# Kernel tuning notes

Measured on AMD Instinct MI355X. Metric: run time of the kernel, lower is better.

Reference implementation:

```python
import jax, jax.numpy as jnp
import numpy as np

R, C = 30, 56
N = R * C  # 1680
K = 0.005
PRCN = 15
ALPHA = 1.0
BETA = 1.0


def setup_inputs() -> dict:
    key = jax.random.key(0)
    k1, k2 = jax.random.split(key)
    net_in = jax.random.normal(k1, (2 * N,), dtype=jnp.float32)
    # Recurrent connectivity matrix (learned weight in the original, loaded from .mat)
    J = jax.random.normal(k2, (N, N), dtype=jnp.float32) / np.float32(np.sqrt(N))
    return {"net_in": net_in, "J": J}


def reference(net_in, J):
    Iext = net_in[:N].reshape(R, C)
    r0 = net_in[N:2 * N].reshape(R, C)

    def step(r, _):
        # 4-way chunked mm + cat in the original == single matvec J @ r_flat
        temp = (J @ r.reshape(N)).reshape(R, C)
        U = ALPHA * (BETA * temp) + ALPHA * Iext
        sq = jnp.square(0.2 * U)
        recSum = jnp.sum(K * sq)
        # (0.2*U)^2 * (0.04 / recSum) / 0.04  ==  sq / recSum, kept explicit for fidelity
        r_new = sq * (0.04 / recSum) / 0.04
        return r_new, (U, recSum)

    r_last, (Us, sums) = jax.lax.scan(step, r0, None, length=PRCN - 1)
    return Us[-1], sums[-1], r_last
```

## Files before the change

### kernel.cpp

```cpp
#include <hip/hip_runtime.h>


typedef float f32x4 __attribute__((ext_vector_type(4)));

#define N      1680
#define NV4    420
#define NSTEP  14
#define GBLK   105
#define RPB    16
#define RPW    4

__device__ __forceinline__ f32x4 llc_load4(const f32x4* p) {
    f32x4 v;
    asm volatile("global_load_dwordx4 %0, %1, off sc0 sc1\n\t"
                 "s_waitcnt vmcnt(0)"
                 : "=v"(v) : "v"(p) : "memory");
    return v;
}
__device__ __forceinline__ void llc_store4(f32x4* p, f32x4 v) {
    asm volatile("global_store_dwordx4 %0, %1, off sc0 sc1"
                 :: "v"(p), "v"(v) : "memory");
}

__global__ __launch_bounds__(256, 1) void fused_recur(
    const float* __restrict__ J,
    const float* __restrict__ net_in,
    float* __restrict__ out,
    float* __restrict__ ws)
{
    __shared__ f32x4 r_lds[NV4];
    __shared__ float sred[4];

    f32x4* bufs = (f32x4*)ws;

    const int tid  = threadIdx.x;
    const int lane = tid & 63;
    const int wave = tid >> 6;
    const int row0 = (int)blockIdx.x * RPB + wave * RPW;

    f32x4 Jr[RPW][7];
    #pragma unroll
    for (int m = 0; m < RPW; ++m) {
        const f32x4* Jrow = (const f32x4*)(J + (size_t)(row0 + m) * N);
        #pragma unroll
        for (int k = 0; k < 7; ++k) {
            const int idx = lane + 64 * k;
            Jr[m][k] = (idx < NV4) ? Jrow[idx] : (f32x4)0.f;
        }
    }
    #pragma unroll
    for (int m = 0; m < RPW; ++m)
        #pragma unroll
        for (int k = 0; k < 7; ++k)
            asm volatile("" : "+v"(Jr[m][k]));

    float iext[RPW];
    #pragma unroll
    for (int m = 0; m < RPW; ++m) iext[m] = net_in[row0 + m];

    float Uv[RPW], Qv[RPW];

    {
        const f32x4* r0 = (const f32x4*)(net_in + N);
        for (int i = tid; i < NV4; i += 256) r_lds[i] = r0[i];
    }
    __syncthreads();
    float s_prev = 1.0f;

    #pragma unroll 1
    for (int t = 0; t < NSTEP; ++t) {
        if (t > 0) {
            f32x4* src = bufs + (size_t)(t - 1) * NV4;
            f32x4 v0 = (f32x4)0.f, v1 = (f32x4)0.f;
            float psum;
            {
                const f32x4* p0 = src + tid;
                do { v0 = llc_load4(p0); }
                while (!(v0[0] >= 0.f && v0[1] >= 0.f &&
                         v0[2] >= 0.f && v0[3] >= 0.f));
                psum = (v0[0] + v0[1]) + (v0[2] + v0[3]);
            }
            const int i1 = tid + 256;
            if (i1 < NV4) {
                const f32x4* p1 = src + i1;
                do { v1 = llc_load4(p1); }
                while (!(v1[0] >= 0.f && v1[1] >= 0.f &&
                         v1[2] >= 0.f && v1[3] >= 0.f));
                psum += (v1[0] + v1[1]) + (v1[2] + v1[3]);
            }
            #pragma unroll
            for (int off = 32; off; off >>= 1) psum += __shfl_xor(psum, off, 64);
            if (lane == 0) sred[wave] = psum;
            r_lds[tid] = v0;
            if (i1 < NV4) r_lds[i1] = v1;
            __syncthreads();
            s_prev = 0.005f * ((sred[0] + sred[1]) + (sred[2] + sred[3]));
        }

        f32x4 rv[7];
        #pragma unroll
        for (int k = 0; k < 7; ++k) {
            const int idx = lane + 64 * k;
            rv[k] = (idx < NV4) ? r_lds[idx] : (f32x4)0.f;
        }

        float a[RPW];
        #pragma unroll
        for (int m = 0; m < RPW; ++m) {
            float acc = 0.f;
            #pragma unroll
            for (int k = 0; k < 7; ++k) {
                acc += Jr[m][k][0] * rv[k][0];
                acc += Jr[m][k][1] * rv[k][1];
                acc += Jr[m][k][2] * rv[k][2];
                acc += Jr[m][k][3] * rv[k][3];
            }
            a[m] = acc;
        }
        #pragma unroll
        for (int off = 32; off; off >>= 1) {
            #pragma unroll
            for (int m = 0; m < RPW; ++m) a[m] += __shfl_xor(a[m], off, 64);
        }

        #pragma unroll
        for (int m = 0; m < RPW; ++m) {
            const float U  = a[m] / s_prev + iext[m];
            const float u2 = 0.2f * U;
            Uv[m] = U;
            Qv[m] = u2 * u2;
        }

        if (lane == 0) {
            f32x4 q4 = { Qv[0], Qv[1], Qv[2], Qv[3] };
            llc_store4(bufs + (size_t)t * NV4 + (row0 >> 2), q4);
        }
        __syncthreads();
    }

    {
        f32x4* src = bufs + (size_t)(NSTEP - 1) * NV4;
        f32x4 v0;
        float psum;
        {
            const f32x4* p0 = src + tid;
            do { v0 = llc_load4(p0); }
            while (!(v0[0] >= 0.f && v0[1] >= 0.f &&
                     v0[2] >= 0.f && v0[3] >= 0.f));
            psum = (v0[0] + v0[1]) + (v0[2] + v0[3]);
        }
        const int i1 = tid + 256;
        if (i1 < NV4) {
            const f32x4* p1 = src + i1;
            f32x4 v1;
            do { v1 = llc_load4(p1); }
            while (!(v1[0] >= 0.f && v1[1] >= 0.f &&
                     v1[2] >= 0.f && v1[3] >= 0.f));
            psum += (v1[0] + v1[1]) + (v1[2] + v1[3]);
        }
        #pragma unroll
        for (int off = 32; off; off >>= 1) psum += __shfl_xor(psum, off, 64);
        if (lane == 0) sred[wave] = psum;
        __syncthreads();
    }
    const float s13 = 0.005f * ((sred[0] + sred[1]) + (sred[2] + sred[3]));

    if (lane == 0) {
        f32x4 u4 = { Uv[0], Uv[1], Uv[2], Uv[3] };
        *(f32x4*)(out + row0) = u4;
    }
    if (lane < RPW) {
        const float q = (lane == 0) ? Qv[0] : (lane == 1) ? Qv[1]
                       : (lane == 2) ? Qv[2] : Qv[3];
        out[N + 1 + row0 + lane] = q / s13;
    }
    if (blockIdx.x == 0 && tid == 0) out[N] = s13;
}

extern "C" void kernel_launch(void* const* d_in, const int* in_sizes, int n_in,
                              void* d_out, int out_size, void* d_ws, size_t ws_size,
                              hipStream_t stream) {
    const float* net_in = (const float*)d_in[0];
    const float* J      = (const float*)d_in[1];
    hipMemsetAsync(d_ws, 0xBF, (size_t)NSTEP * NV4 * sizeof(f32x4), stream);
    fused_recur<<<GBLK, 256, 0, stream>>>(J, net_in, (float*)d_out, (float*)d_ws);
}
```

Baseline: 109.3 us.

## Poll full r-vector per wave directly from global, dropping LDS and block barriers

Each wave now polls all 420 vectors of the previous step's published state straight from global memory with seven batched uncached loads and a single wait. It computes the normalising sum itself and folds that reduction into the existing matvec shuffle reduction. This removes the LDS staging and both __syncthreads per step, so waves in a block proceed independently. The cost is four times more polling traffic per block to the shared cache, and a retry now reloads all seven vectors whenever any element is not yet ready.

After: 117.1 us. 7.1% more time.

```diff
diff --git a/kernel.cpp b/kernel.cpp
--- a/kernel.cpp
+++ b/kernel.cpp
@@ -10,16 +10,37 @@
 #define RPB    16
 #define RPW    4
 
-__device__ __forceinline__ f32x4 llc_load4(const f32x4* p) {
-    f32x4 v;
-    asm volatile("global_load_dwordx4 %0, %1, off sc0 sc1\n\t"
-                 "s_waitcnt vmcnt(0)"
-                 : "=v"(v) : "v"(p) : "memory");
-    return v;
-}
+__device__ __forceinline__ void load7_llc(
+    const f32x4* p0, const f32x4* p1, const f32x4* p2, const f32x4* p3,
+    const f32x4* p4, const f32x4* p5, const f32x4* p6,
+    f32x4& v0, f32x4& v1, f32x4& v2, f32x4& v3,
+    f32x4& v4, f32x4& v5, f32x4& v6)
+{
+    asm volatile(
+        "global_load_dwordx4 %0, %7, off sc0 sc1\n\t"
+        "global_load_dwordx4 %1, %8, off sc0 sc1\n\t"
+        "global_load_dwordx4 %2, %9, off sc0 sc1\n\t"
+        "global_load_dwordx4 %3, %10, off sc0 sc1\n\t"
+        "global_load_dwordx4 %4, %11, off sc0 sc1\n\t"
+        "global_load_dwordx4 %5, %12, off sc0 sc1\n\t"
+        "global_load_dwordx4 %6, %13, off sc0 sc1\n\t"
+        "s_waitcnt vmcnt(0)"
+        : "=&v"(v0), "=&v"(v1), "=&v"(v2), "=&v"(v3),
+          "=&v"(v4), "=&v"(v5), "=&v"(v6)
+        : "v"(p0), "v"(p1), "v"(p2), "v"(p3), "v"(p4), "v"(p5), "v"(p6)
+        : "memory");
+}
+
 __device__ __forceinline__ void llc_store4(f32x4* p, f32x4 v) {
     asm volatile("global_store_dwordx4 %0, %1, off sc0 sc1"
                  :: "v"(p), "v"(v) : "memory");
+}
+
+__device__ __forceinline__ f32x4 vmin4(f32x4 a, f32x4 b) {
+    f32x4 r;
+    r[0] = fminf(a[0], b[0]); r[1] = fminf(a[1], b[1]);
+    r[2] = fminf(a[2], b[2]); r[3] = fminf(a[3], b[3]);
+    return r;
 }
 
 __global__ __launch_bounds__(256, 1) void fused_recur(
@@ -28,9 +49,6 @@
     float* __restrict__ out,
     float* __restrict__ ws)
 {
-    __shared__ f32x4 r_lds[NV4];
-    __shared__ float sred[4];
-
     f32x4* bufs = (f32x4*)ws;
 
     const int tid  = threadIdx.x;
@@ -48,11 +66,6 @@
             Jr[m][k] = (idx < NV4) ? Jrow[idx] : (f32x4)0.f;
         }
     }
-    #pragma unroll
-    for (int m = 0; m < RPW; ++m)
-        #pragma unroll
-        for (int k = 0; k < 7; ++k)
-            asm volatile("" : "+v"(Jr[m][k]));
 
     float iext[RPW];
     #pragma unroll
@@ -60,51 +73,49 @@
 
     float Uv[RPW], Qv[RPW];
 
-    {
-        const f32x4* r0 = (const f32x4*)(net_in + N);
-        for (int i = tid; i < NV4; i += 256) r_lds[i] = r0[i];
-    }
-    __syncthreads();
-    float s_prev = 1.0f;
-
     #pragma unroll 1
     for (int t = 0; t < NSTEP; ++t) {
-        if (t > 0) {
-            f32x4* src = bufs + (size_t)(t - 1) * NV4;
-            f32x4 v0 = (f32x4)0.f, v1 = (f32x4)0.f;
-            float psum;
-            {
-                const f32x4* p0 = src + tid;
-                do { v0 = llc_load4(p0); }
-                while (!(v0[0] >= 0.f && v0[1] >= 0.f &&
-                         v0[2] >= 0.f && v0[3] >= 0.f));
-                psum = (v0[0] + v0[1]) + (v0[2] + v0[3]);
+        #pragma unroll
+        for (int m = 0; m < RPW; ++m)
+            #pragma unroll
+            for (int k = 0; k < 7; ++k)
+                asm volatile("" : "+v"(Jr[m][k]));
+
+        f32x4 rv[7];
+        float psum = 0.0f;
+
+        if (t == 0) {
+            const f32x4* r0 = (const f32x4*)(net_in + N);
+            #pragma unroll
+            for (int k = 0; k < 7; ++k) {
+                const int idx = lane + 64 * k;
+                rv[k] = (idx < NV4) ? r0[idx] : (f32x4)0.f;
             }
-            const int i1 = tid + 256;
-            if (i1 < NV4) {
-                const f32x4* p1 = src + i1;
-                do { v1 = llc_load4(p1); }
-                while (!(v1[0] >= 0.f && v1[1] >= 0.f &&
-                         v1[2] >= 0.f && v1[3] >= 0.f));
-                psum += (v1[0] + v1[1]) + (v1[2] + v1[3]);
+        } else {
+            const f32x4* base = bufs + (size_t)(t - 1) * NV4;
+            const f32x4* q0 = base + (lane);
+            const f32x4* q1 = base + (lane + 64);
+            const f32x4* q2 = base + (lane + 128);
+            const f32x4* q3 = base + (lane + 192);
+            const f32x4* q4 = base + (lane + 256);
+            const f32x4* q5 = base + (lane + 320);
+            const f32x4* q6 = (lane < 36) ? (base + lane + 384) : base;
+            for (;;) {
+                load7_llc(q0, q1, q2, q3, q4, q5, q6,
+                          rv[0], rv[1], rv[2], rv[3], rv[4], rv[5], rv[6]);
+                f32x4 m0 = vmin4(vmin4(rv[0], rv[1]), vmin4(rv[2], rv[3]));
+                f32x4 m1 = vmin4(vmin4(rv[4], rv[5]), rv[6]);
+                f32x4 mm = vmin4(m0, m1);
+                const float mn = fminf(fminf(mm[0], mm[1]), fminf(mm[2], mm[3]));
+                if (mn >= 0.0f) break;
             }
-            #pragma unroll
-            for (int off = 32; off; off >>= 1) psum += __shfl_xor(psum, off, 64);
-            if (lane == 0) sred[wave] = psum;
-            r_lds[tid] = v0;
-            if (i1 < NV4) r_lds[i1] = v1;
-            __syncthreads();
-            s_prev = 0.005f * ((sred[0] + sred[1]) + (sred[2] + sred[3]));
-        }
-
-        f32x4 rv[7];
-        #pragma unroll
-        for (int k = 0; k < 7; ++k) {
-            const int idx = lane + 64 * k;
-            rv[k] = (idx < NV4) ? r_lds[idx] : (f32x4)0.f;
-        }
-
-        float a[RPW];
+            if (lane >= 36) rv[6] = (f32x4)0.f;
+            #pragma unroll
+            for (int k = 0; k < 7; ++k)
+                psum += (rv[k][0] + rv[k][1]) + (rv[k][2] + rv[k][3]);
+        }
+
+        float red[5];
         #pragma unroll
         for (int m = 0; m < RPW; ++m) {
             float acc = 0.f;
@@ -115,55 +126,59 @@
                 acc += Jr[m][k][2] * rv[k][2];
                 acc += Jr[m][k][3] * rv[k][3];
             }
-            a[m] = acc;
-        }
+            red[m] = acc;
+        }
+        red[4] = psum;
         #pragma unroll
         for (int off = 32; off; off >>= 1) {
             #pragma unroll
-            for (int m = 0; m < RPW; ++m) a[m] += __shfl_xor(a[m], off, 64);
-        }
+            for (int i = 0; i < 5; ++i) red[i] += __shfl_xor(red[i], off, 64);
+        }
+        const float s = (t == 0) ? 1.0f : 0.005f * red[4];
 
         #pragma unroll
         for (int m = 0; m < RPW; ++m) {
-            const float U  = a[m] / s_prev + iext[m];
+            const float U  = red[m] / s + iext[m];
             const float u2 = 0.2f * U;
             Uv[m] = U;
             Qv[m] = u2 * u2;
         }
 
         if (lane == 0) {
-            f32x4 q4 = { Qv[0], Qv[1], Qv[2], Qv[3] };
-            llc_store4(bufs + (size_t)t * NV4 + (row0 >> 2), q4);
-        }
-        __syncthreads();
-    }
-
+            f32x4 pub = { Qv[0], Qv[1], Qv[2], Qv[3] };
+            llc_store4(bufs + (size_t)t * NV4 + (row0 >> 2), pub);
+        }
+    }
+
+    float s13;
     {
-        f32x4* src = bufs + (size_t)(NSTEP - 1) * NV4;
-        f32x4 v0;
-        float psum;
-        {
-            const f32x4* p0 = src + tid;
-            do { v0 = llc_load4(p0); }
-            while (!(v0[0] >= 0.f && v0[1] >= 0.f &&
-                     v0[2] >= 0.f && v0[3] >= 0.f));
-            psum = (v0[0] + v0[1]) + (v0[2] + v0[3]);
-        }
-        const int i1 = tid + 256;
-        if (i1 < NV4) {
-            const f32x4* p1 = src + i1;
-            f32x4 v1;
-            do { v1 = llc_load4(p1); }
-            while (!(v1[0] >= 0.f && v1[1] >= 0.f &&
-                     v1[2] >= 0.f && v1[3] >= 0.f));
-            psum += (v1[0] + v1[1]) + (v1[2] + v1[3]);
-        }
+        const f32x4* base = bufs + (size_t)(NSTEP - 1) * NV4;
+        const f32x4* q0 = base + (lane);
+        const f32x4* q1 = base + (lane + 64);
+        const f32x4* q2 = base + (lane + 128);
+        const f32x4* q3 = base + (lane + 192);
+        const f32x4* q4 = base + (lane + 256);
+        const f32x4* q5 = base + (lane + 320);
+        const f32x4* q6 = (lane < 36) ? (base + lane + 384) : base;
+        f32x4 rv[7];
+        for (;;) {
+            load7_llc(q0, q1, q2, q3, q4, q5, q6,
+                      rv[0], rv[1], rv[2], rv[3], rv[4], rv[5], rv[6]);
+            f32x4 m0 = vmin4(vmin4(rv[0], rv[1]), vmin4(rv[2], rv[3]));
+            f32x4 m1 = vmin4(vmin4(rv[4], rv[5]), rv[6]);
+            f32x4 mm = vmin4(m0, m1);
+            const float mn = fminf(fminf(mm[0], mm[1]), fminf(mm[2], mm[3]));
+            if (mn >= 0.0f) break;
+        }
+        if (lane >= 36) rv[6] = (f32x4)0.f;
+        float psum = 0.f;
+        #pragma unroll
+        for (int k = 0; k < 7; ++k)
+            psum += (rv[k][0] + rv[k][1]) + (rv[k][2] + rv[k][3]);
         #pragma unroll
         for (int off = 32; off; off >>= 1) psum += __shfl_xor(psum, off, 64);
-        if (lane == 0) sred[wave] = psum;
-        __syncthreads();
-    }
-    const float s13 = 0.005f * ((sred[0] + sred[1]) + (sred[2] + sred[3]));
+        s13 = 0.005f * psum;
+    }
 
     if (lane == 0) {
         f32x4 u4 = { Uv[0], Uv[1], Uv[2], Uv[3] };
```

## Stream J from cache each step, use fewer larger blocks with double-buffered LDS

Applied to the files above, without the earlier changes.

Stops keeping the J rows in registers. Each step now reads them from global memory (cache), and the launch uses 35 blocks of 768 threads instead of 105 blocks of 256. The recSum reduction is folded into the matvec wave reduction, so every wave computes the sum itself and the shared-memory cross-wave reduction goes away. The next r vector is polled into a double-buffered LDS slot within the same step, which leaves one barrier per step. This lowers register pressure and the number of blocks that must synchronise through global memory. In exchange, about 11 MB of J must be re-read from cache or HBM on every step.

Result: slower. 154.1 us (+40.9%).

```diff
diff --git a/kernel.cpp b/kernel.cpp
--- a/kernel.cpp
+++ b/kernel.cpp
@@ -6,8 +6,9 @@
 #define N      1680
 #define NV4    420
 #define NSTEP  14
-#define GBLK   105
-#define RPB    16
+#define GBLK   35
+#define NTHR   768
+#define RPB    48
 #define RPW    4
 
 __device__ __forceinline__ f32x4 llc_load4(const f32x4* p) {
@@ -22,14 +23,13 @@
                  :: "v"(p), "v"(v) : "memory");
 }
 
-__global__ __launch_bounds__(256, 1) void fused_recur(
+__global__ __launch_bounds__(NTHR, 3) void fused_recur(
     const float* __restrict__ J,
     const float* __restrict__ net_in,
     float* __restrict__ out,
     float* __restrict__ ws)
 {
-    __shared__ f32x4 r_lds[NV4];
-    __shared__ float sred[4];
+    __shared__ f32x4 lds_r[2][NV4];
 
     f32x4* bufs = (f32x4*)ws;
 
@@ -38,132 +38,101 @@
     const int wave = tid >> 6;
     const int row0 = (int)blockIdx.x * RPB + wave * RPW;
 
-    f32x4 Jr[RPW][7];
-    #pragma unroll
-    for (int m = 0; m < RPW; ++m) {
-        const f32x4* Jrow = (const f32x4*)(J + (size_t)(row0 + m) * N);
-        #pragma unroll
-        for (int k = 0; k < 7; ++k) {
-            const int idx = lane + 64 * k;
-            Jr[m][k] = (idx < NV4) ? Jrow[idx] : (f32x4)0.f;
-        }
-    }
-    #pragma unroll
-    for (int m = 0; m < RPW; ++m)
-        #pragma unroll
-        for (int k = 0; k < 7; ++k)
-            asm volatile("" : "+v"(Jr[m][k]));
-
     float iext[RPW];
     #pragma unroll
     for (int m = 0; m < RPW; ++m) iext[m] = net_in[row0 + m];
 
+    const f32x4* jb[RPW];
+    #pragma unroll
+    for (int m = 0; m < RPW; ++m)
+        jb[m] = (const f32x4*)(J + (size_t)(row0 + m) * N);
+
     float Uv[RPW], Qv[RPW];
 
-    {
-        const f32x4* r0 = (const f32x4*)(net_in + N);
-        for (int i = tid; i < NV4; i += 256) r_lds[i] = r0[i];
-    }
+    if (tid < NV4) lds_r[0][tid] = ((const f32x4*)(net_in + N))[tid];
     __syncthreads();
-    float s_prev = 1.0f;
 
     #pragma unroll 1
     for (int t = 0; t < NSTEP; ++t) {
-        if (t > 0) {
-            f32x4* src = bufs + (size_t)(t - 1) * NV4;
-            f32x4 v0 = (f32x4)0.f, v1 = (f32x4)0.f;
-            float psum;
-            {
-                const f32x4* p0 = src + tid;
-                do { v0 = llc_load4(p0); }
-                while (!(v0[0] >= 0.f && v0[1] >= 0.f &&
-                         v0[2] >= 0.f && v0[3] >= 0.f));
-                psum = (v0[0] + v0[1]) + (v0[2] + v0[3]);
-            }
-            const int i1 = tid + 256;
-            if (i1 < NV4) {
-                const f32x4* p1 = src + i1;
-                do { v1 = llc_load4(p1); }
-                while (!(v1[0] >= 0.f && v1[1] >= 0.f &&
-                         v1[2] >= 0.f && v1[3] >= 0.f));
-                psum += (v1[0] + v1[1]) + (v1[2] + v1[3]);
-            }
-            #pragma unroll
-            for (int off = 32; off; off >>= 1) psum += __shfl_xor(psum, off, 64);
-            if (lane == 0) sred[wave] = psum;
-            r_lds[tid] = v0;
-            if (i1 < NV4) r_lds[i1] = v1;
-            __syncthreads();
-            s_prev = 0.005f * ((sred[0] + sred[1]) + (sred[2] + sred[3]));
-        }
+        const f32x4* src = lds_r[t & 1];
 
         f32x4 rv[7];
         #pragma unroll
         for (int k = 0; k < 7; ++k) {
             const int idx = lane + 64 * k;
-            rv[k] = (idx < NV4) ? r_lds[idx] : (f32x4)0.f;
+            rv[k] = (idx < NV4) ? src[idx] : (f32x4)0.f;
         }
 
-        float a[RPW];
+        f32x4 acc[RPW];
         #pragma unroll
-        for (int m = 0; m < RPW; ++m) {
-            float acc = 0.f;
-            #pragma unroll
-            for (int k = 0; k < 7; ++k) {
-                acc += Jr[m][k][0] * rv[k][0];
-                acc += Jr[m][k][1] * rv[k][1];
-                acc += Jr[m][k][2] * rv[k][2];
-                acc += Jr[m][k][3] * rv[k][3];
+        for (int m = 0; m < RPW; ++m) acc[m] = (f32x4)0.f;
+        float psum = 0.0f;
+        #pragma unroll
+        for (int k = 0; k < 7; ++k) {
+            const int idx = lane + 64 * k;
+            if (idx < NV4) {
+                #pragma unroll
+                for (int m = 0; m < RPW; ++m) {
+                    const f32x4 a = jb[m][idx];
+                    acc[m][0] += a[0] * rv[k][0];
+                    acc[m][1] += a[1] * rv[k][1];
+                    acc[m][2] += a[2] * rv[k][2];
+                    acc[m][3] += a[3] * rv[k][3];
+                }
+                psum += (rv[k][0] + rv[k][1]) + (rv[k][2] + rv[k][3]);
             }
-            a[m] = acc;
         }
+
+        float red[5];
+        #pragma unroll
+        for (int m = 0; m < RPW; ++m)
+            red[m] = (acc[m][0] + acc[m][1]) + (acc[m][2] + acc[m][3]);
+        red[4] = psum;
         #pragma unroll
         for (int off = 32; off; off >>= 1) {
             #pragma unroll
-            for (int m = 0; m < RPW; ++m) a[m] += __shfl_xor(a[m], off, 64);
+            for (int i = 0; i < 5; ++i) red[i] += __shfl_xor(red[i], off, 64);
         }
+        const float inv = (t == 0) ? 1.0f : 1.0f / (0.005f * red[4]);
 
         #pragma unroll
         for (int m = 0; m < RPW; ++m) {
-            const float U  = a[m] / s_prev + iext[m];
+            const float U  = red[m] * inv + iext[m];
             const float u2 = 0.2f * U;
             Uv[m] = U;
             Qv[m] = u2 * u2;
         }
 
         if (lane == 0) {
-            f32x4 q4 = { Qv[0], Qv[1], Qv[2], Qv[3] };
-            llc_store4(bufs + (size_t)t * NV4 + (row0 >> 2), q4);
+            f32x4 pub = { Qv[0], Qv[1], Qv[2], Qv[3] };
+            llc_store4(bufs + (size_t)t * NV4 + (row0 >> 2), pub);
+        }
+
+        if (tid < NV4) {
+            const f32x4* p = bufs + (size_t)t * NV4 + tid;
+            f32x4 v;
+            do { v = llc_load4(p); }
+            while (!(v[0] >= 0.f && v[1] >= 0.f && v[2] >= 0.f && v[3] >= 0.f));
+            lds_r[(t + 1) & 1][tid] = v;
         }
         __syncthreads();
     }
 
+    float psum = 0.0f;
     {
-        f32x4* src = bufs + (size_t)(NSTEP - 1) * NV4;
-        f32x4 v0;
-        float psum;
-        {
-            const f32x4* p0 = src + tid;
-            do { v0 = llc_load4(p0); }
-            while (!(v0[0] >= 0.f && v0[1] >= 0.f &&
-                     v0[2] >= 0.f && v0[3] >= 0.f));
-            psum = (v0[0] + v0[1]) + (v0[2] + v0[3]);
+        const f32x4* src = lds_r[0];
+        #pragma unroll
+        for (int k = 0; k < 7; ++k) {
+            const int idx = lane + 64 * k;
+            if (idx < NV4) {
+                const f32x4 q = src[idx];
+                psum += (q[0] + q[1]) + (q[2] + q[3]);
+            }
         }
-        const int i1 = tid + 256;
-        if (i1 < NV4) {
-            const f32x4* p1 = src + i1;
-            f32x4 v1;
-            do { v1 = llc_load4(p1); }
-            while (!(v1[0] >= 0.f && v1[1] >= 0.f &&
-                     v1[2] >= 0.f && v1[3] >= 0.f));
-            psum += (v1[0] + v1[1]) + (v1[2] + v1[3]);
-        }
-        #pragma unroll
-        for (int off = 32; off; off >>= 1) psum += __shfl_xor(psum, off, 64);
-        if (lane == 0) sred[wave] = psum;
-        __syncthreads();
     }
-    const float s13 = 0.005f * ((sred[0] + sred[1]) + (sred[2] + sred[3]));
+    #pragma unroll
+    for (int off = 32; off; off >>= 1) psum += __shfl_xor(psum, off, 64);
+    const float s13 = 0.005f * psum;
 
     if (lane == 0) {
         f32x4 u4 = { Uv[0], Uv[1], Uv[2], Uv[3] };
@@ -183,5 +152,5 @@
     const float* net_in = (const float*)d_in[0];
     const float* J      = (const float*)d_in[1];
     hipMemsetAsync(d_ws, 0xBF, (size_t)NSTEP * NV4 * sizeof(f32x4), stream);
-    fused_recur<<<GBLK, 256, 0, stream>>>(J, net_in, (float*)d_out, (float*)d_ws);
+    fused_recur<<<GBLK, NTHR, 0, stream>>>(J, net_in, (float*)d_out, (float*)d_ws);
 }
```
